# Kernel optimization log

Measured on AMD Instinct MI355X. Metric: run time of the kernel, lower is better.

## Reference

```python
import jax, jax.numpy as jnp
import numpy as np

EPS = 1e-5

def _layer_norm_12(x):
    # Normalization('layer'): mean/var over dims (1,2), torch.var is unbiased (ddof=1)
    mean = x.mean(axis=(1, 2), keepdims=True)
    n = x.shape[1] * x.shape[2]
    var = ((x - mean) ** 2).sum(axis=(1, 2), keepdims=True) / (n - 1)
    return (x - mean) / jnp.sqrt(var + EPS)

def setup_inputs() -> dict:
    key = jax.random.key(0)
    ks = jax.random.split(key, 14)
    B, N, D, H, FF = 64, 256, 128, 8, 512
    dk = D // H  # key_dim == val_dim == 16
    u = lambda k, shape, fan: jax.random.uniform(k, shape, jnp.float32, -1.0, 1.0) / np.sqrt(fan)
    return {
        "h_em": jax.random.normal(ks[0], (B, N, D), jnp.float32),
        "route_attn": jax.random.normal(ks[1], (H, B, N, N), jnp.float32),
        "Wq": u(ks[2], (H, D, dk), dk),
        "Wk": u(ks[3], (H, D, dk), dk),
        "Wv": u(ks[4], (H, D, dk), dk),
        "W_out": u(ks[5], (H, dk, D), D),
        "sa_w1": u(ks[6], (2 * H, 2 * H), 2 * H),   # score_aggr Linear1 (in,out)
        "sa_b1": u(ks[7], (2 * H,), 2 * H),
        "sa_w2": u(ks[8], (2 * H, H), H),           # score_aggr Linear2 (in,out)
        "sa_b2": u(ks[9], (H,), H),
        "ff_w1": u(ks[10], (D, FF), FF),
        "ff_w2": u(ks[11], (FF, D), D),
    }

def reference(h_em, route_attn, Wq, Wk, Wv, W_out, sa_w1, sa_b1, sa_w2, sa_b2, ff_w1, ff_w2):
    # ---- SynthAtt ----
    Q = jnp.einsum('bnd,hdk->hbnk', h_em, Wq)
    K = jnp.einsum('bnd,hdk->hbnk', h_em, Wk)
    V = jnp.einsum('bnd,hdv->hbnv', h_em, Wv)
    scores = jnp.einsum('hbnk,hbmk->hbnm', Q, K)            # no 1/sqrt(dk) scaling (faithful)
    compat = jnp.concatenate([scores, route_attn], axis=0)  # [2H, B, N, N]
    mixed = compat.transpose(1, 2, 3, 0)                    # [B, N, N, 2H]
    hdn = jax.nn.relu(mixed @ sa_w1 + sa_b1)
    attn = (hdn @ sa_w2 + sa_b2).transpose(3, 0, 1, 2)      # [H, B, N, N]
    soft = jax.nn.softmax(attn, axis=-1)
    heads = jnp.einsum('hbnm,hbmv->hbnv', soft, V)          # [H, B, N, dk]
    out = jnp.einsum('hbnv,hvd->bnd', heads, W_out)         # concat-heads @ W_out
    # ---- MHA sublayer norm ----
    x = _layer_norm_12(out + h_em)
    # ---- FF + Norm sublayer ----
    ff = jax.nn.relu(x @ ff_w1) @ ff_w2
    out1 = _layer_norm_12(ff + x)
    return (out1, route_attn)
```

## Files before the change

### kernel.cpp

```cpp
#include <hip/hip_runtime.h>
#include <hip/hip_bf16.h>

typedef __bf16 bf16x8 __attribute__((ext_vector_type(8)));
typedef float  f32x4  __attribute__((ext_vector_type(4)));

#define DEVI __device__ __forceinline__

DEVI float bf2f(__hip_bfloat16 x) { return __bfloat162float(x); }
DEVI __hip_bfloat16 f2bf(float x) { return __float2bfloat16(x); }

DEVI f32x4 mfma16(bf16x8 a, bf16x8 b, f32x4 c) {
    return __builtin_amdgcn_mfma_f32_16x16x32_bf16(a, b, c, 0, 0, 0);
}

DEVI bf16x8 ld8(const __hip_bfloat16* p) {
    return *reinterpret_cast<const bf16x8*>(p);
}

DEVI bf16x8 cvt8(const float* p) {
    bf16x8 r;
#pragma unroll
    for (int i = 0; i < 8; ++i) r[i] = (__bf16)p[i];
    return r;
}

DEVI unsigned cvtpk(float a, float b) {
    unsigned r;
    asm("v_cvt_pk_bf16_f32 %0, %1, %2" : "=v"(r) : "v"(a), "v"(b));
    return r;
}

DEVI bf16x8 u4bf(unsigned x0, unsigned x1, unsigned x2, unsigned x3) {
    union { unsigned u[4]; bf16x8 b; } cv;
    cv.u[0] = x0; cv.u[1] = x1; cv.u[2] = x2; cv.u[3] = x3;
    return cv.b;
}


__global__ __launch_bounds__(256) void repack_kernel(
    const float* __restrict__ Wq, const float* __restrict__ Wk,
    const float* __restrict__ Wv, const float* __restrict__ W_out,
    const float* __restrict__ ff_w1, const float* __restrict__ ff_w2,
    __hip_bfloat16* __restrict__ Wqkvt, __hip_bfloat16* __restrict__ Wot,
    __hip_bfloat16* __restrict__ w1t, __hip_bfloat16* __restrict__ w2t)
{
    int t = blockIdx.x * 256 + threadIdx.x;
    if (t < 49152) {
        int c = t >> 7, d = t & 127;
        int qkv = c >> 7, h = (c >> 4) & 7, k = c & 15;
        const float* W = (qkv == 0) ? Wq : (qkv == 1) ? Wk : Wv;
        Wqkvt[t] = f2bf(W[(h * 128 + d) * 16 + k]);
    } else if (t < 65536) {
        int idx = t - 49152;
        int d = idx >> 7, hv = idx & 127, h = hv >> 4, v = hv & 15;
        Wot[idx] = f2bf(W_out[(h * 16 + v) * 128 + d]);
    } else if (t < 131072) {
        int idx = t - 65536;
        int f = idx >> 7, d = idx & 127;
        w1t[idx] = f2bf(ff_w1[d * 512 + f]);
    } else {
        int idx = t - 131072;
        int d2 = idx >> 9, f = idx & 511;
        w2t[idx] = f2bf(ff_w2[f * 128 + d2]);
    }
}

__global__ __launch_bounds__(512) void qkv_kernel(
    const float* __restrict__ hem, const __hip_bfloat16* __restrict__ Wqkvt,
    __hip_bfloat16* __restrict__ Qb, __hip_bfloat16* __restrict__ Kb,
    __hip_bfloat16* __restrict__ Vtb)
{
    const int w = threadIdx.x >> 6, lane = threadIdx.x & 63;
    const int quad = lane >> 4, col = lane & 15;
    const int row0 = blockIdx.x * 32;

    f32x4 acc[2][3] = {};
#pragma unroll
    for (int ks = 0; ks < 4; ++ks) {
        bf16x8 a[2], bb[3];
#pragma unroll
        for (int mt = 0; mt < 2; ++mt)
            a[mt] = cvt8(hem + (size_t)(row0 + mt * 16 + col) * 128 + ks * 32 + quad * 8);
#pragma unroll
        for (int nt = 0; nt < 3; ++nt) {
            int c = (w * 3 + nt) * 16 + col;
            bb[nt] = ld8(Wqkvt + (size_t)c * 128 + ks * 32 + quad * 8);
        }
#pragma unroll
        for (int mt = 0; mt < 2; ++mt)
#pragma unroll
            for (int nt = 0; nt < 3; ++nt)
                acc[mt][nt] = mfma16(a[mt], bb[nt], acc[mt][nt]);
    }
#pragma unroll
    for (int mt = 0; mt < 2; ++mt)
#pragma unroll
        for (int nt = 0; nt < 3; ++nt)
#pragma unroll
            for (int rg = 0; rg < 4; ++rg) {
                int row = row0 + mt * 16 + quad * 4 + rg;
                int c = (w * 3 + nt) * 16 + col;
                int qkv = c >> 7, h = (c >> 4) & 7, k = c & 15;
                int bb_ = row >> 8, n = row & 255;
                __hip_bfloat16 v = f2bf(acc[mt][nt][rg]);
                if (qkv == 0)      Qb[(((size_t)bb_ * 8 + h) * 256 + n) * 16 + k] = v;
                else if (qkv == 1) Kb[(((size_t)bb_ * 8 + h) * 256 + n) * 16 + k] = v;
                else               Vtb[(((size_t)bb_ * 8 + h) * 16 + k) * 256 + n] = v;
            }
}

__global__ __launch_bounds__(512) void attn_kernel_v4(
    const __hip_bfloat16* __restrict__ Qb, const __hip_bfloat16* __restrict__ Kb,
    const __hip_bfloat16* __restrict__ Vtb, const float* __restrict__ route,
    const float* __restrict__ sa_w1, const float* __restrict__ sa_b1,
    const float* __restrict__ sa_w2, const float* __restrict__ sa_b2,
    const float* __restrict__ h_em, const __hip_bfloat16* __restrict__ Wot,
    float* __restrict__ y, float* __restrict__ out)
{
    __shared__ alignas(16) __hip_bfloat16 srb[2 * 2048 * 8 + 8];
    __shared__ alignas(16) __hip_bfloat16 headsb[8][144];
    __shared__ alignas(16) __hip_bfloat16 saw1t[16][32];
    __shared__ alignas(16) __hip_bfloat16 saw2t[16][32];
    __shared__ float b1s[16], b2s[16];
    __hip_bfloat16* sb = srb;
    __hip_bfloat16* rb = srb + 16384 + 8;
    float* sbf = reinterpret_cast<float*>(sb);
    float* rbf = reinterpret_cast<float*>(rb);

    const int tid = threadIdx.x;
    const int w = tid >> 6, lane = tid & 63, quad = lane >> 4, col = lane & 15;
    const int b = blockIdx.x >> 5, tile = blockIdx.x & 31, n0 = tile * 8;
    const f32x4 zero = {0.f, 0.f, 0.f, 0.f};

    {
        int o = tid >> 5, i = tid & 31;
        saw1t[o][i] = (i < 16) ? f2bf(sa_w1[i * 16 + o]) : f2bf(0.f);
        saw2t[o][i] = (i < 16 && o < 8) ? f2bf(sa_w2[i * 8 + o]) : f2bf(0.f);
        if (tid < 16) {
            b1s[tid] = sa_b1[tid];
            b2s[tid] = (tid < 8) ? sa_b2[tid] : 0.f;
        }
    }

    {
        const int h = w;
        const size_t rbase = (((size_t)h * 64 + b) * 256 + n0) * 256;
        const float* rsrc = route + rbase;
        float rv[32];
#pragma unroll
        for (int r = 0; r < 8; ++r)
#pragma unroll
            for (int j = 0; j < 4; ++j)
                rv[r * 4 + j] = rsrc[r * 256 + j * 64 + lane];

        const __hip_bfloat16* Qh = Qb + ((size_t)(b * 8 + h)) * 256 * 16;
        const __hip_bfloat16* Kh = Kb + ((size_t)(b * 8 + h)) * 256 * 16;
        bf16x8 aq = ld8(Qh + (size_t)(n0 + (col & 7)) * 16 + (quad & 1) * 8);
#pragma unroll
        for (int nt = 0; nt < 16; ++nt) {
            bf16x8 bk = {};
            if (quad < 2) bk = ld8(Kh + (size_t)(nt * 16 + col) * 16 + quad * 8);
            f32x4 c = mfma16(aq, bk, zero);
            if (quad < 2) {
#pragma unroll
                for (int rg = 0; rg < 4; ++rg)
                    sb[((quad * 4 + rg) * 256 + nt * 16 + col) * 8 + h] = f2bf(c[rg]);
            }
        }
        float* rdst = out + 2097152 + rbase;
#pragma unroll
        for (int r = 0; r < 8; ++r)
#pragma unroll
            for (int j = 0; j < 4; ++j) {
                int nm = r * 256 + j * 64 + lane;
                float v = rv[r * 4 + j];
                rdst[nm] = v;
                rb[nm * 8 + h] = f2bf(v);
            }
    }
    __syncthreads();

    {
        bf16x8 a1 = ld8(&saw1t[col][quad * 8]);
        bf16x8 a2 = ld8(&saw2t[col][quad * 8]);
        f32x4 bv1 = *(const f32x4*)&b1s[quad * 4];
        f32x4 bv2 = *(const f32x4*)&b2s[quad * 4];
        const __hip_bfloat16* arow = (quad & 1) ? rb : sb;
        float* dstf = quad ? rbf : sbf;
        const int rowbase = w * 256 + col;
        const int src0 = (lane & 15) + ((lane >> 4) & 1) * 32;

        bf16x8 b1 = ld8(&arow[(size_t)rowbase * 8]);
#pragma unroll
        for (int t8 = 0; t8 < 16; ++t8) {
            f32x4 c1 = mfma16(a1, b1, zero);
            bf16x8 b1n = b1;
            if (t8 < 15) b1n = ld8(&arow[(size_t)(rowbase + (t8 + 1) * 16) * 8]);
            unsigned p0 = cvtpk(fmaxf(c1[0] + bv1[0], 0.f), fmaxf(c1[1] + bv1[1], 0.f));
            unsigned p1 = cvtpk(fmaxf(c1[2] + bv1[2], 0.f), fmaxf(c1[3] + bv1[3], 0.f));
            unsigned x0 = __shfl((int)p0, src0, 64);
            unsigned x1 = __shfl((int)p1, src0, 64);
            unsigned x2 = __shfl((int)p0, src0 + 16, 64);
            unsigned x3 = __shfl((int)p1, src0 + 16, 64);
            bf16x8 b2 = u4bf(x0, x1, x2, x3);
            f32x4 c2 = mfma16(a2, b2, zero);
            if (quad < 2) {
                int base = (w * 256 + t8 * 16 + col) * 4;
#pragma unroll
                for (int rg = 0; rg < 4; ++rg)
                    dstf[base + rg] = c2[rg] + bv2[rg];
            }
            b1 = b1n;
        }
    }
    __syncthreads();

    float vv[32];
    {
        const float* src = (w < 4) ? sbf : rbf;
        const int c = w & 3;
#pragma unroll
        for (int r = 0; r < 8; ++r)
#pragma unroll
            for (int j = 0; j < 4; ++j)
                vv[r * 4 + j] = src[(r * 256 + j * 64 + lane) * 4 + c];
    }
    __syncthreads();

    {
        char* softw = (char*)srb + w * 4096;
#pragma unroll
        for (int r = 0; r < 8; ++r) {
            float v0 = vv[r * 4], v1 = vv[r * 4 + 1], v2 = vv[r * 4 + 2], v3 = vv[r * 4 + 3];
            float mx = fmaxf(fmaxf(v0, v1), fmaxf(v2, v3));
#pragma unroll
            for (int off = 32; off; off >>= 1) mx = fmaxf(mx, __shfl_xor(mx, off, 64));
            float e0 = __expf(v0 - mx), e1 = __expf(v1 - mx);
            float e2 = __expf(v2 - mx), e3 = __expf(v3 - mx);
            float s = e0 + e1 + e2 + e3;
#pragma unroll
            for (int off = 32; off; off >>= 1) s += __shfl_xor(s, off, 64);
            float inv = 1.f / s;
            char* rowp = softw + r * 512;
            const int swz = r << 4;
            *(__hip_bfloat16*)(rowp + (((0 * 64 + lane) * 2) ^ swz)) = f2bf(e0 * inv);
            *(__hip_bfloat16*)(rowp + (((1 * 64 + lane) * 2) ^ swz)) = f2bf(e1 * inv);
            *(__hip_bfloat16*)(rowp + (((2 * 64 + lane) * 2) ^ swz)) = f2bf(e2 * inv);
            *(__hip_bfloat16*)(rowp + (((3 * 64 + lane) * 2) ^ swz)) = f2bf(e3 * inv);
        }
    }

    {
        const int h = w;
        f32x4 acc = zero;
        const __hip_bfloat16* Vh = Vtb + ((size_t)(b * 8 + h)) * 16 * 256;
        const char* softh = (const char*)srb + h * 4096 + (col & 7) * 512;
        const int sx = (col & 7) << 4;
#pragma unroll
        for (int ks = 0; ks < 8; ++ks) {
            bf16x8 a = *(const bf16x8*)(softh + ((ks * 64 + quad * 16) ^ sx));
            bf16x8 bv = ld8(Vh + (size_t)col * 256 + ks * 32 + quad * 8);
            acc = mfma16(a, bv, acc);
        }
        if (quad < 2) {
#pragma unroll
            for (int rg = 0; rg < 4; ++rg)
                headsb[quad * 4 + rg][h * 16 + col] = f2bf(acc[rg]);
        }
    }
    __syncthreads();

    {
        f32x4 acc = zero;
#pragma unroll
        for (int ks = 0; ks < 4; ++ks) {
            bf16x8 a = *(const bf16x8*)&headsb[col & 7][ks * 32 + quad * 8];
            bf16x8 bo = ld8(Wot + (size_t)(w * 16 + col) * 128 + ks * 32 + quad * 8);
            acc = mfma16(a, bo, acc);
        }
        if (quad < 2) {
#pragma unroll
            for (int rg = 0; rg < 4; ++rg) {
                int n = n0 + quad * 4 + rg, d = w * 16 + col;
                size_t idx = ((size_t)b * 256 + n) * 128 + d;
                y[idx] = acc[rg] + h_em[idx];
            }
        }
    }
}

DEVI void stout(float* p, float v) { *p = v; }
DEVI void stout(__hip_bfloat16* p, float v) { *p = f2bf(v); }

template<typename OUT>
__global__ __launch_bounds__(1024) void ln_kernel(
    const float* __restrict__ y, OUT* __restrict__ out)
{
    const int b = blockIdx.x;
    const float* yb = y + (size_t)b * 32768;
    float v[32], s = 0.f, sq = 0.f;
#pragma unroll
    for (int j = 0; j < 32; ++j) {
        float x = yb[threadIdx.x + 1024 * j];
        v[j] = x; s += x; sq += x * x;
    }
#pragma unroll
    for (int off = 32; off; off >>= 1) {
        s += __shfl_down(s, off, 64);
        sq += __shfl_down(sq, off, 64);
    }
    __shared__ float ps[16], pq[16], stats[2];
    int wv = threadIdx.x >> 6, ln = threadIdx.x & 63;
    if (ln == 0) { ps[wv] = s; pq[wv] = sq; }
    __syncthreads();
    if (threadIdx.x < 64) {
        float a = (ln < 16) ? ps[ln] : 0.f;
        float bq = (ln < 16) ? pq[ln] : 0.f;
#pragma unroll
        for (int off = 8; off; off >>= 1) {
            a += __shfl_down(a, off, 64);
            bq += __shfl_down(bq, off, 64);
        }
        if (ln == 0) {
            float mean = a * (1.f / 32768.f);
            float var = fmaxf((bq - 32768.f * mean * mean) * (1.f / 32767.f), 0.f);
            stats[0] = mean;
            stats[1] = rsqrtf(var + 1e-5f);
        }
    }
    __syncthreads();
    float mean = stats[0], rstd = stats[1];
    OUT* ob = out + (size_t)b * 32768;
#pragma unroll
    for (int j = 0; j < 32; ++j)
        stout(ob + threadIdx.x + 1024 * j, (v[j] - mean) * rstd);
}

__global__ __launch_bounds__(512) void ff_kernel(
    const __hip_bfloat16* __restrict__ xb, const __hip_bfloat16* __restrict__ w1t,
    const __hip_bfloat16* __restrict__ w2t, float* __restrict__ y)
{
    __shared__ alignas(16) __hip_bfloat16 hid[64][512];
    const int w = threadIdx.x >> 6, lane = threadIdx.x & 63;
    const int quad = lane >> 4, col = lane & 15;
    const int r0 = blockIdx.x * 64;

    f32x4 acc[4][4] = {};
#pragma unroll
    for (int ks = 0; ks < 4; ++ks) {
        bf16x8 a[4], bb[4];
#pragma unroll
        for (int mt = 0; mt < 4; ++mt)
            a[mt] = ld8(xb + (size_t)(r0 + mt * 16 + col) * 128 + ks * 32 + quad * 8);
#pragma unroll
        for (int nt = 0; nt < 4; ++nt) {
            int f = (w * 4 + nt) * 16 + col;
            bb[nt] = ld8(w1t + (size_t)f * 128 + ks * 32 + quad * 8);
        }
#pragma unroll
        for (int mt = 0; mt < 4; ++mt)
#pragma unroll
            for (int nt = 0; nt < 4; ++nt)
                acc[mt][nt] = mfma16(a[mt], bb[nt], acc[mt][nt]);
    }
#pragma unroll
    for (int mt = 0; mt < 4; ++mt)
#pragma unroll
        for (int nt = 0; nt < 4; ++nt)
#pragma unroll
            for (int rg = 0; rg < 4; ++rg) {
                int row = mt * 16 + quad * 4 + rg;
                int f = (w * 4 + nt) * 16 + col;
                hid[row][f] = f2bf(fmaxf(acc[mt][nt][rg], 0.f));
            }
    __syncthreads();

    f32x4 acc2[4] = {};
#pragma unroll
    for (int ks = 0; ks < 16; ++ks) {
        bf16x8 bb = ld8(w2t + (size_t)(w * 16 + col) * 512 + ks * 32 + quad * 8);
#pragma unroll
        for (int mt = 0; mt < 4; ++mt) {
            bf16x8 a = *(const bf16x8*)&hid[mt * 16 + col][ks * 32 + quad * 8];
            acc2[mt] = mfma16(a, bb, acc2[mt]);
        }
    }
#pragma unroll
    for (int mt = 0; mt < 4; ++mt)
#pragma unroll
        for (int rg = 0; rg < 4; ++rg) {
            int row = r0 + mt * 16 + quad * 4 + rg;
            int d = w * 16 + col;
            size_t idx = (size_t)row * 128 + d;
            y[idx] = acc2[mt][rg] + bf2f(xb[idx]);
        }
}

extern "C" void kernel_launch(void* const* d_in, const int* in_sizes, int n_in,
                              void* d_out, int out_size, void* d_ws, size_t ws_size,
                              hipStream_t stream)
{
    const float* h_em  = (const float*)d_in[0];
    const float* route = (const float*)d_in[1];
    const float* Wq    = (const float*)d_in[2];
    const float* Wk    = (const float*)d_in[3];
    const float* Wv    = (const float*)d_in[4];
    const float* W_out = (const float*)d_in[5];
    const float* sa_w1 = (const float*)d_in[6];
    const float* sa_b1 = (const float*)d_in[7];
    const float* sa_w2 = (const float*)d_in[8];
    const float* sa_b2 = (const float*)d_in[9];
    const float* ff_w1 = (const float*)d_in[10];
    const float* ff_w2 = (const float*)d_in[11];

    char* ws = (char*)d_ws;
    __hip_bfloat16* Qb    = (__hip_bfloat16*)(ws);
    __hip_bfloat16* Kb    = (__hip_bfloat16*)(ws + 4194304);
    __hip_bfloat16* Vtb   = (__hip_bfloat16*)(ws + 8388608);
    __hip_bfloat16* Wqkvt = (__hip_bfloat16*)(ws + 12582912);
    __hip_bfloat16* Wot   = (__hip_bfloat16*)(ws + 12681216);
    __hip_bfloat16* w1t   = (__hip_bfloat16*)(ws + 12713984);
    __hip_bfloat16* w2t   = (__hip_bfloat16*)(ws + 12845056);
    float*          yv    = (float*)(ws + 12976128);
    __hip_bfloat16* xb    = (__hip_bfloat16*)(ws + 21364736);

    hipLaunchKernelGGL(repack_kernel, dim3(768), dim3(256), 0, stream,
                       Wq, Wk, Wv, W_out, ff_w1, ff_w2, Wqkvt, Wot, w1t, w2t);
    hipLaunchKernelGGL(qkv_kernel, dim3(512), dim3(512), 0, stream,
                       h_em, Wqkvt, Qb, Kb, Vtb);
    hipLaunchKernelGGL(attn_kernel_v4, dim3(2048), dim3(512), 0, stream,
                       Qb, Kb, Vtb, route, sa_w1, sa_b1, sa_w2, sa_b2, h_em, Wot,
                       yv, (float*)d_out);
    hipLaunchKernelGGL(ln_kernel<__hip_bfloat16>, dim3(64), dim3(1024), 0, stream, yv, xb);
    hipLaunchKernelGGL(ff_kernel, dim3(256), dim3(512), 0, stream, xb, w1t, w2t, yv);
    hipLaunchKernelGGL(ln_kernel<float>, dim3(64), dim3(1024), 0, stream,
                       yv, (float*)d_out);
}
```

Measured before the change: 375.6 us.

## Keep score-aggregation logits in registers and fuse softmax without LDS round trip

```diff
diff --git a/kernel.cpp b/kernel.cpp
--- a/kernel.cpp
+++ b/kernel.cpp
@@ -2,6 +2,7 @@
 #include <hip/hip_bf16.h>
 
 typedef __bf16 bf16x8 __attribute__((ext_vector_type(8)));
+typedef __bf16 bf16x4 __attribute__((ext_vector_type(4)));
 typedef float  f32x4  __attribute__((ext_vector_type(4)));
 
 #define DEVI __device__ __forceinline__
@@ -18,9 +19,11 @@
 }
 
 DEVI bf16x8 cvt8(const float* p) {
+    f32x4 u = *reinterpret_cast<const f32x4*>(p);
+    f32x4 v = *reinterpret_cast<const f32x4*>(p + 4);
     bf16x8 r;
-#pragma unroll
-    for (int i = 0; i < 8; ++i) r[i] = (__bf16)p[i];
+    r[0] = (__bf16)u[0]; r[1] = (__bf16)u[1]; r[2] = (__bf16)u[2]; r[3] = (__bf16)u[3];
+    r[4] = (__bf16)v[0]; r[5] = (__bf16)v[1]; r[6] = (__bf16)v[2]; r[7] = (__bf16)v[3];
     return r;
 }
 
@@ -34,6 +37,12 @@
     union { unsigned u[4]; bf16x8 b; } cv;
     cv.u[0] = x0; cv.u[1] = x1; cv.u[2] = x2; cv.u[3] = x3;
     return cv.b;
+}
+
+DEVI bf16x8 pad4(bf16x4 v) {
+    bf16x8 r = {};
+    r[0] = v[0]; r[1] = v[1]; r[2] = v[2]; r[3] = v[3];
+    return r;
 }
 
 
@@ -109,7 +118,7 @@
             }
 }
 
-__global__ __launch_bounds__(512) void attn_kernel_v4(
+__global__ __launch_bounds__(512, 4) void attn_kernel_v5(
     const __hip_bfloat16* __restrict__ Qb, const __hip_bfloat16* __restrict__ Kb,
     const __hip_bfloat16* __restrict__ Vtb, const float* __restrict__ route,
     const float* __restrict__ sa_w1, const float* __restrict__ sa_b1,
@@ -119,27 +128,25 @@
 {
     __shared__ alignas(16) __hip_bfloat16 srb[2 * 2048 * 8 + 8];
     __shared__ alignas(16) __hip_bfloat16 headsb[8][144];
-    __shared__ alignas(16) __hip_bfloat16 saw1t[16][32];
-    __shared__ alignas(16) __hip_bfloat16 saw2t[16][32];
-    __shared__ float b1s[16], b2s[16];
+    __shared__ alignas(16) __hip_bfloat16 saw1t16[16][16];
+    __shared__ alignas(16) __hip_bfloat16 saw2t16[16][16];
+    __shared__ float b1s[16];
     __hip_bfloat16* sb = srb;
     __hip_bfloat16* rb = srb + 16384 + 8;
-    float* sbf = reinterpret_cast<float*>(sb);
-    float* rbf = reinterpret_cast<float*>(rb);
 
     const int tid = threadIdx.x;
     const int w = tid >> 6, lane = tid & 63, quad = lane >> 4, col = lane & 15;
+    const int quad4 = quad * 4;
     const int b = blockIdx.x >> 5, tile = blockIdx.x & 31, n0 = tile * 8;
     const f32x4 zero = {0.f, 0.f, 0.f, 0.f};
 
     {
-        int o = tid >> 5, i = tid & 31;
-        saw1t[o][i] = (i < 16) ? f2bf(sa_w1[i * 16 + o]) : f2bf(0.f);
-        saw2t[o][i] = (i < 16 && o < 8) ? f2bf(sa_w2[i * 8 + o]) : f2bf(0.f);
-        if (tid < 16) {
-            b1s[tid] = sa_b1[tid];
-            b2s[tid] = (tid < 8) ? sa_b2[tid] : 0.f;
-        }
+        if (tid < 256) {
+            int o = tid >> 4, i = tid & 15;
+            saw1t16[o][i] = f2bf(sa_w1[i * 16 + o]);
+            saw2t16[o][i] = (o < 8) ? f2bf(sa_w2[i * 8 + o]) : f2bf(0.f);
+        }
+        if (tid < 16) b1s[tid] = sa_b1[tid];
     }
 
     {
@@ -180,75 +187,64 @@
     }
     __syncthreads();
 
-    {
-        bf16x8 a1 = ld8(&saw1t[col][quad * 8]);
-        bf16x8 a2 = ld8(&saw2t[col][quad * 8]);
-        f32x4 bv1 = *(const f32x4*)&b1s[quad * 4];
-        f32x4 bv2 = *(const f32x4*)&b2s[quad * 4];
-        const __hip_bfloat16* arow = (quad & 1) ? rb : sb;
-        float* dstf = quad ? rbf : sbf;
-        const int rowbase = w * 256 + col;
-        const int src0 = (lane & 15) + ((lane >> 4) & 1) * 32;
-
-        bf16x8 b1 = ld8(&arow[(size_t)rowbase * 8]);
+    float lg[4][16];
+    {
+        bf16x8 a1 = pad4(*(const bf16x4*)&saw1t16[col][quad4]);
+        bf16x8 a2 = pad4(*(const bf16x4*)&saw2t16[col][quad4]);
+        f32x4 bv1 = *(const f32x4*)&b1s[quad4];
+        const char* aptr = (const char*)((quad & 2) ? rb : sb) + (quad & 1) * 8;
+        const int rowbase = (w * 256 + col) * 16;
+
+        bf16x4 b4 = *(const bf16x4*)(aptr + rowbase);
 #pragma unroll
         for (int t8 = 0; t8 < 16; ++t8) {
+            bf16x8 b1 = pad4(b4);
+            if (t8 < 15) b4 = *(const bf16x4*)(aptr + rowbase + (t8 + 1) * 256);
             f32x4 c1 = mfma16(a1, b1, zero);
-            bf16x8 b1n = b1;
-            if (t8 < 15) b1n = ld8(&arow[(size_t)(rowbase + (t8 + 1) * 16) * 8]);
-            unsigned p0 = cvtpk(fmaxf(c1[0] + bv1[0], 0.f), fmaxf(c1[1] + bv1[1], 0.f));
-            unsigned p1 = cvtpk(fmaxf(c1[2] + bv1[2], 0.f), fmaxf(c1[3] + bv1[3], 0.f));
-            unsigned x0 = __shfl((int)p0, src0, 64);
-            unsigned x1 = __shfl((int)p1, src0, 64);
-            unsigned x2 = __shfl((int)p0, src0 + 16, 64);
-            unsigned x3 = __shfl((int)p1, src0 + 16, 64);
-            bf16x8 b2 = u4bf(x0, x1, x2, x3);
-            f32x4 c2 = mfma16(a2, b2, zero);
-            if (quad < 2) {
-                int base = (w * 256 + t8 * 16 + col) * 4;
-#pragma unroll
-                for (int rg = 0; rg < 4; ++rg)
-                    dstf[base + rg] = c2[rg] + bv2[rg];
-            }
-            b1 = b1n;
-        }
-    }
-    __syncthreads();
-
-    float vv[32];
-    {
-        const float* src = (w < 4) ? sbf : rbf;
-        const int c = w & 3;
-#pragma unroll
-        for (int r = 0; r < 8; ++r)
-#pragma unroll
-            for (int j = 0; j < 4; ++j)
-                vv[r * 4 + j] = src[(r * 256 + j * 64 + lane) * 4 + c];
-    }
-    __syncthreads();
-
-    {
-        char* softw = (char*)srb + w * 4096;
-#pragma unroll
-        for (int r = 0; r < 8; ++r) {
-            float v0 = vv[r * 4], v1 = vv[r * 4 + 1], v2 = vv[r * 4 + 2], v3 = vv[r * 4 + 3];
-            float mx = fmaxf(fmaxf(v0, v1), fmaxf(v2, v3));
-#pragma unroll
-            for (int off = 32; off; off >>= 1) mx = fmaxf(mx, __shfl_xor(mx, off, 64));
-            float e0 = __expf(v0 - mx), e1 = __expf(v1 - mx);
-            float e2 = __expf(v2 - mx), e3 = __expf(v3 - mx);
-            float s = e0 + e1 + e2 + e3;
-#pragma unroll
-            for (int off = 32; off; off >>= 1) s += __shfl_xor(s, off, 64);
-            float inv = 1.f / s;
-            char* rowp = softw + r * 512;
-            const int swz = r << 4;
-            *(__hip_bfloat16*)(rowp + (((0 * 64 + lane) * 2) ^ swz)) = f2bf(e0 * inv);
-            *(__hip_bfloat16*)(rowp + (((1 * 64 + lane) * 2) ^ swz)) = f2bf(e1 * inv);
-            *(__hip_bfloat16*)(rowp + (((2 * 64 + lane) * 2) ^ swz)) = f2bf(e2 * inv);
-            *(__hip_bfloat16*)(rowp + (((3 * 64 + lane) * 2) ^ swz)) = f2bf(e3 * inv);
-        }
-    }
+            unsigned q0 = cvtpk(fmaxf(c1[0] + bv1[0], 0.f), fmaxf(c1[1] + bv1[1], 0.f));
+            unsigned q1 = cvtpk(fmaxf(c1[2] + bv1[2], 0.f), fmaxf(c1[3] + bv1[3], 0.f));
+            f32x4 c2 = mfma16(a2, u4bf(q0, q1, 0, 0), zero);
+#pragma unroll
+            for (int rg = 0; rg < 4; ++rg) lg[rg][t8] = c2[rg];
+        }
+    }
+
+    float inv[4];
+    {
+#pragma unroll
+        for (int rg = 0; rg < 4; ++rg) {
+            float mx = lg[rg][0];
+#pragma unroll
+            for (int t = 1; t < 16; ++t) mx = fmaxf(mx, lg[rg][t]);
+#pragma unroll
+            for (int off = 1; off < 16; off <<= 1) mx = fmaxf(mx, __shfl_xor(mx, off, 64));
+            float s = 0.f;
+#pragma unroll
+            for (int t = 0; t < 16; ++t) {
+                float e = __expf(lg[rg][t] - mx);
+                lg[rg][t] = e; s += e;
+            }
+#pragma unroll
+            for (int off = 1; off < 16; off <<= 1) s += __shfl_xor(s, off, 64);
+            inv[rg] = 1.f / s;
+        }
+    }
+    __syncthreads();
+
+    {
+        if (quad < 2) {
+            const int swz = w << 4;
+#pragma unroll
+            for (int rg = 0; rg < 4; ++rg) {
+                char* slab = (char*)srb + (quad4 + rg) * 4096 + w * 512;
+                float iv = inv[rg];
+#pragma unroll
+                for (int t = 0; t < 16; ++t)
+                    *(__hip_bfloat16*)(slab + (((t * 16 + col) * 2) ^ swz)) = f2bf(lg[rg][t] * iv);
+            }
+        }
+    }
+    __syncthreads();
 
     {
         const int h = w;
@@ -340,7 +336,7 @@
     const __hip_bfloat16* __restrict__ xb, const __hip_bfloat16* __restrict__ w1t,
     const __hip_bfloat16* __restrict__ w2t, float* __restrict__ y)
 {
-    __shared__ alignas(16) __hip_bfloat16 hid[64][512];
+    __shared__ alignas(16) __hip_bfloat16 hid[64][520];
     const int w = threadIdx.x >> 6, lane = threadIdx.x & 63;
     const int quad = lane >> 4, col = lane & 15;
     const int r0 = blockIdx.x * 64;
@@ -428,7 +424,7 @@
                        Wq, Wk, Wv, W_out, ff_w1, ff_w2, Wqkvt, Wot, w1t, w2t);
     hipLaunchKernelGGL(qkv_kernel, dim3(512), dim3(512), 0, stream,
                        h_em, Wqkvt, Qb, Kb, Vtb);
-    hipLaunchKernelGGL(attn_kernel_v4, dim3(2048), dim3(512), 0, stream,
+    hipLaunchKernelGGL(attn_kernel_v5, dim3(2048), dim3(512), 0, stream,
                        Qb, Kb, Vtb, route, sa_w1, sa_b1, sa_w2, sa_b2, h_em, Wot,
                        yv, (float*)d_out);
     hipLaunchKernelGGL(ln_kernel<__hip_bfloat16>, dim3(64), dim3(1024), 0, stream, yv, xb);
```

Measured after the change: 354.6 us. 5.6% less time.
